# Kernel optimization log

Measured on AMD Instinct MI355X. Metric: run time of the kernel, lower is better.

## Reference

```python
import jax, jax.numpy as jnp
import numpy as np

D_MODEL = 256; N_HEADS = 8; N_LEVELS = 4; N_POINTS = 4
D_HEAD = D_MODEL // N_HEADS


def setup_inputs() -> dict:
    key = jax.random.key(0)
    ks = jax.random.split(key, 8)
    N, Lq = 4, 4096
    shapes = np.array([4096, 2048, 1024, 512], dtype=np.int32)  # temporal lengths per level
    Len_in = int(shapes.sum())  # 7680
    start = np.concatenate([[0], np.cumsum(shapes)[:-1]]).astype(np.int32)
    HLP = N_HEADS * N_LEVELS * N_POINTS
    return {
        "query": jax.random.normal(ks[0], (N, Lq, D_MODEL), jnp.float32),
        "reference_points": jax.random.uniform(ks[1], (N, Lq, N_LEVELS, 1), jnp.float32),
        "input_flatten": jax.random.normal(ks[2], (N, Len_in, D_MODEL), jnp.float32),
        "input_spatial_shapes": jnp.asarray(shapes),
        "input_level_start_index": jnp.asarray(start),
        "W_off": jax.random.normal(ks[3], (D_MODEL, HLP), jnp.float32) * 0.01,
        "b_off": jax.random.normal(ks[4], (HLP,), jnp.float32) * 2.0,
        "W_aw": jax.random.normal(ks[5], (D_MODEL, HLP), jnp.float32) * 0.02,
        "b_aw": jnp.zeros((HLP,), jnp.float32),
        "W_v": jax.random.normal(ks[6], (D_MODEL, D_MODEL), jnp.float32) / np.sqrt(D_MODEL).astype(np.float32),
        "b_v": jnp.zeros((D_MODEL,), jnp.float32),
        "W_out": jax.random.normal(ks[7], (D_MODEL, D_MODEL), jnp.float32) / np.sqrt(D_MODEL).astype(np.float32),
        "b_out": jnp.zeros((D_MODEL,), jnp.float32),
    }


def reference(query, reference_points, input_flatten, input_spatial_shapes,
              input_level_start_index, W_off, b_off, W_aw, b_aw, W_v, b_v,
              W_out, b_out):
    N, Lq, C = query.shape
    M, L, P, Dh = N_HEADS, N_LEVELS, N_POINTS, D_HEAD
    S = input_flatten.shape[1]

    value = (input_flatten @ W_v + b_v).reshape(N, S, M, Dh)
    off = (query @ W_off + b_off).reshape(N, Lq, M, L, P)
    aw = jax.nn.softmax((query @ W_aw + b_aw).reshape(N, Lq, M, L * P), axis=-1)
    aw = aw.reshape(N, Lq, M, L, P)

    # reference_points last dim == 1 branch: loc = ref + off / T_l, in [0,1]
    T = input_spatial_shapes.astype(jnp.float32)[None, None, None, :, None]  # [1,1,1,L,1]
    loc = reference_points[:, :, None, :, None, 0] + off / T  # [N,Lq,M,L,P]

    # grid_sample(align_corners=False, padding_mode='border') along W with H=1, y=0.5:
    # pixel coord x = loc*T - 0.5, clamped to [0, T-1], then linear interp.
    x = jnp.clip(loc * T - 0.5, 0.0, T - 1.0)
    x0 = jnp.floor(x)
    w1 = x - x0                                   # frac weight for right neighbor
    i0 = x0.astype(jnp.int32)
    i1 = jnp.minimum(i0 + 1, input_spatial_shapes[None, None, None, :, None] - 1)
    base = input_level_start_index[None, None, None, :, None]
    g0 = i0 + base                                # global flattened indices [N,Lq,M,L,P]
    g1 = i1 + base

    v = value.transpose(0, 2, 1, 3)               # [N,M,S,Dh]

    def gather(idx):
        idxt = idx.transpose(0, 2, 1, 3, 4).reshape(N, M, Lq * L * P, 1)
        return jnp.take_along_axis(v, idxt, axis=2).reshape(N, M, Lq, L, P, Dh)

    s0 = gather(g0)
    s1 = gather(g1)
    w1t = w1.transpose(0, 2, 1, 3, 4)[..., None]   # [N,M,Lq,L,P,1]
    samp = s0 * (1.0 - w1t) + s1 * w1t             # [N,M,Lq,L,P,Dh]

    awt = aw.transpose(0, 2, 1, 3, 4)[..., None]
    out = (samp * awt).sum(axis=(3, 4))            # [N,M,Lq,Dh]
    out = out.transpose(0, 2, 1, 3).reshape(N, Lq, M * Dh)
    return out @ W_out + b_out
```

## Files before the change

kernel.cpp:

```cpp
#include <hip/hip_runtime.h>
#include <hip/hip_bf16.h>
#include <cstddef>
#include <cstdint>

#define D_MODEL   256
#define N_HEADS   8
#define N_LEVELS  4
#define N_POINTS  4
#define D_HEAD    32
#define HLP       128
#define NBATCH    4
#define LQ        4096
#define S_LEN     7680

typedef __attribute__((ext_vector_type(8))) short  short8;
typedef __attribute__((ext_vector_type(4))) float  f32x4;
typedef __attribute__((ext_vector_type(8))) unsigned short ushort8;

__device__ __forceinline__ unsigned short f2bf(float x) {
    __hip_bfloat16 h = __float2bfloat16(x);
    return *reinterpret_cast<unsigned short*>(&h);
}
__device__ __forceinline__ float bf2f(unsigned short u) {
    unsigned int v = ((unsigned int)u) << 16;
    return *reinterpret_cast<float*>(&v);
}

__device__ __forceinline__ void gload_lds16(const void* g, void* l) {
    __builtin_amdgcn_global_load_lds(
        (const __attribute__((address_space(1))) void*)g,
        (__attribute__((address_space(3))) void*)l,
        16, 0, 0);
}

__global__ __launch_bounds__(256) void conv_bf16_kernel(
    const float* __restrict__ src, unsigned short* __restrict__ dst, int n)
{
    size_t i = ((size_t)blockIdx.x * blockDim.x + threadIdx.x) * 8;
    if (i >= (size_t)n) return;
    float4 a = *(const float4*)(src + i);
    float4 b = *(const float4*)(src + i + 4);
    ushort8 r;
    r[0] = f2bf(a.x); r[1] = f2bf(a.y); r[2] = f2bf(a.z); r[3] = f2bf(a.w);
    r[4] = f2bf(b.x); r[5] = f2bf(b.y); r[6] = f2bf(b.z); r[7] = f2bf(b.w);
    *(ushort8*)(dst + i) = r;
}

__global__ __launch_bounds__(256) void transpose_w_kernel(
    const float* __restrict__ src, unsigned short* __restrict__ dst, int N)
{
    __shared__ float t[64][65];
    const int k0 = blockIdx.y * 64, n0 = blockIdx.x * 64;
    const int tid = threadIdx.x;
    #pragma unroll
    for (int i = 0; i < 16; ++i) {
        int idx = tid + i * 256;
        int kk = idx >> 6, nn = idx & 63;
        t[kk][nn] = src[(size_t)(k0 + kk) * N + n0 + nn];
    }
    __syncthreads();
    #pragma unroll
    for (int i = 0; i < 16; ++i) {
        int idx = tid + i * 256;
        int nn = idx >> 6, kk = idx & 63;
        dst[(size_t)(n0 + nn) * 256 + k0 + kk] = f2bf(t[kk][nn]);
    }
}

__global__ void bias_cat_kernel(const float* __restrict__ b0,
                                const float* __restrict__ b1,
                                float* __restrict__ out)
{
    int t = threadIdx.x;
    out[t] = (t < 128) ? b0[t] : b1[t - 128];
}

template <bool BF16_OUT>
__global__ __launch_bounds__(256) void mfma_gemm_kernel(
    const unsigned short* __restrict__ A,
    const unsigned short* __restrict__ Bt,
    const float* __restrict__ bias,
    void* __restrict__ Cout, int M)
{
    __shared__ unsigned short Als[8][64][8];
    __shared__ unsigned short Bls[8][64][8];

    const int tid  = threadIdx.x;
    const int lane = tid & 63;
    const int w    = tid >> 6;
    const int wm   = w & 1;
    const int wn   = w >> 1;
    const int row0 = blockIdx.y * 128;
    const int col0 = blockIdx.x * 128;

    const int lr = (lane & 15);
    const int lk = (lane >> 4) * 8;

    f32x4 acc[4][4] = {};

    for (int kt = 0; kt < 8; ++kt) {
        const int k0 = kt * 32;
        #pragma unroll
        for (int c = 0; c < 2; ++c) {
            const int im = w * 2 + c;
            const size_t ga = (size_t)(row0 + im * 16 + lr) * 256 + k0 + lk;
            gload_lds16(A + ga, &Als[im][0][0]);
            const int in = w * 2 + c;
            const size_t gb = (size_t)(col0 + in * 16 + lr) * 256 + k0 + lk;
            gload_lds16(Bt + gb, &Bls[in][0][0]);
        }
        __syncthreads();

        short8 af[4], bfr[4];
        #pragma unroll
        for (int i = 0; i < 4; ++i) af[i]  = *(const short8*)&Als[wm * 4 + i][lane][0];
        #pragma unroll
        for (int j = 0; j < 4; ++j) bfr[j] = *(const short8*)&Bls[wn * 4 + j][lane][0];

        #pragma unroll
        for (int i = 0; i < 4; ++i)
            #pragma unroll
            for (int j = 0; j < 4; ++j)
                acc[i][j] = __builtin_amdgcn_mfma_f32_16x16x32_bf16(
                    af[i], bfr[j], acc[i][j], 0, 0, 0);
        __syncthreads();
    }

    const int r0 = row0 + wm * 64;
    const int c0 = col0 + wn * 64;
    const int prow = (lane >> 4) * 4;
    const int pcol = lane & 15;
    #pragma unroll
    for (int j = 0; j < 4; ++j) {
        const int col = c0 + j * 16 + pcol;
        const float bs = bias[col];
        #pragma unroll
        for (int i = 0; i < 4; ++i) {
            #pragma unroll
            for (int r = 0; r < 4; ++r) {
                const int row = r0 + i * 16 + prow + r;
                const float v = acc[i][j][r] + bs;
                if (BF16_OUT)
                    ((unsigned short*)Cout)[(size_t)row * 256 + col] = f2bf(v);
                else
                    ((float*)Cout)[(size_t)row * 256 + col] = v;
            }
        }
    }
}

__global__ __launch_bounds__(128) void sample_kernel(
    const float* __restrict__ P, const float* __restrict__ refp,
    const int* __restrict__ shapes, const int* __restrict__ lstart,
    const unsigned short* __restrict__ value, unsigned short* __restrict__ tout)
{
    __shared__ int   sg0[HLP];
    __shared__ int   sg1[HLP];
    __shared__ float sw[HLP];
    __shared__ float se[HLP];
    __shared__ float smax[N_HEADS];
    __shared__ float srsum[N_HEADS];

    const int nq  = blockIdx.x;
    const int n   = nq >> 12;
    const int tid = threadIdx.x;

    {
        const int l = (tid >> 2) & 3;
        const float off   = P[(size_t)nq * 256 + tid];
        const float logit = P[(size_t)nq * 256 + 128 + tid];
        const float T     = (float)shapes[l];
        const float ref   = refp[(size_t)nq * N_LEVELS + l];
        float x = ref * T + off - 0.5f;
        x = fminf(fmaxf(x, 0.0f), T - 1.0f);
        const float x0 = floorf(x);
        const int   i0 = (int)x0;
        const int   i1 = min(i0 + 1, shapes[l] - 1);
        const int   base = lstart[l];
        sg0[tid] = i0 + base;
        sg1[tid] = i1 + base;
        sw[tid]  = x - x0;
        se[tid]  = logit;
    }
    __syncthreads();
    if (tid < N_HEADS) {
        float mx = -1e30f;
        #pragma unroll
        for (int i = 0; i < 16; ++i) mx = fmaxf(mx, se[tid * 16 + i]);
        smax[tid] = mx;
    }
    __syncthreads();
    se[tid] = __expf(se[tid] - smax[tid >> 4]);
    __syncthreads();
    if (tid < N_HEADS) {
        float s = 0.f;
        #pragma unroll
        for (int i = 0; i < 16; ++i) s += se[tid * 16 + i];
        srsum[tid] = 1.0f / s;
    }
    __syncthreads();

    const int m  = tid >> 4;
    const int dp = tid & 15;
    const float rs = srsum[m];
    const unsigned short* vbase = value + (size_t)n * S_LEN * 256 + m * 32 + 2 * dp;

    float acc0 = 0.f, acc1 = 0.f;
    #pragma unroll
    for (int i = 0; i < 16; ++i) {
        const int j = m * 16 + i;
        const float a = se[j] * rs;
        const float ww = sw[j];
        const unsigned int u0 = *(const unsigned int*)(vbase + (size_t)sg0[j] * 256);
        const unsigned int u1 = *(const unsigned int*)(vbase + (size_t)sg1[j] * 256);
        const float v0a = bf2f((unsigned short)(u0 & 0xffff));
        const float v0b = bf2f((unsigned short)(u0 >> 16));
        const float v1a = bf2f((unsigned short)(u1 & 0xffff));
        const float v1b = bf2f((unsigned short)(u1 >> 16));
        acc0 += a * (v0a + ww * (v1a - v0a));
        acc1 += a * (v0b + ww * (v1b - v0b));
    }
    unsigned int out = (unsigned int)f2bf(acc0) | ((unsigned int)f2bf(acc1) << 16);
    *(unsigned int*)(tout + (size_t)nq * 256 + 2 * tid) = out;
}

extern "C" void kernel_launch(void* const* d_in, const int* in_sizes, int n_in,
                              void* d_out, int out_size, void* d_ws, size_t ws_size,
                              hipStream_t stream)
{
    const float* query  = (const float*)d_in[0];
    const float* refp   = (const float*)d_in[1];
    const float* inflat = (const float*)d_in[2];
    const int*   shapes = (const int*)d_in[3];
    const int*   lstart = (const int*)d_in[4];
    const float* W_off  = (const float*)d_in[5];
    const float* b_off  = (const float*)d_in[6];
    const float* W_aw   = (const float*)d_in[7];
    const float* b_aw   = (const float*)d_in[8];
    const float* W_v    = (const float*)d_in[9];
    const float* b_v    = (const float*)d_in[10];
    const float* W_out  = (const float*)d_in[11];
    const float* b_out  = (const float*)d_in[12];

    const int M_val = NBATCH * S_LEN;
    const int M_q   = NBATCH * LQ;
    const int n_val = M_val * D_MODEL;
    const int n_q   = M_q * D_MODEL;

    char* p = (char*)d_ws;
    unsigned short* value_bf  = (unsigned short*)p; p += (size_t)n_val * 2;
    float*          P         = (float*)p;          p += (size_t)M_q * 256 * 4;
    unsigned short* inflat_bf = (unsigned short*)p; p += (size_t)n_val * 2;
    unsigned short* query_bf  = (unsigned short*)p; p += (size_t)n_q * 2;
    unsigned short* tbuf      = query_bf;
    unsigned short* Wv_t      = (unsigned short*)p; p += 256 * 256 * 2;
    unsigned short* Wcat_t    = (unsigned short*)p; p += 256 * 256 * 2;
    unsigned short* Wout_t    = (unsigned short*)p; p += 256 * 256 * 2;
    float*          bcat      = (float*)p;          p += 256 * 4;

    conv_bf16_kernel<<<(n_val / 8 + 255) / 256, 256, 0, stream>>>(inflat, inflat_bf, n_val);
    conv_bf16_kernel<<<(n_q / 8 + 255) / 256, 256, 0, stream>>>(query, query_bf, n_q);
    transpose_w_kernel<<<dim3(4, 4), 256, 0, stream>>>(W_v, Wv_t, 256);
    transpose_w_kernel<<<dim3(2, 4), 256, 0, stream>>>(W_off, Wcat_t, 128);
    transpose_w_kernel<<<dim3(2, 4), 256, 0, stream>>>(W_aw, Wcat_t + 128 * 256, 128);
    transpose_w_kernel<<<dim3(4, 4), 256, 0, stream>>>(W_out, Wout_t, 256);
    bias_cat_kernel<<<1, 256, 0, stream>>>(b_off, b_aw, bcat);

    mfma_gemm_kernel<true><<<dim3(2, M_val / 128), 256, 0, stream>>>(
        inflat_bf, Wv_t, b_v, value_bf, M_val);
    mfma_gemm_kernel<false><<<dim3(2, M_q / 128), 256, 0, stream>>>(
        query_bf, Wcat_t, bcat, P, M_q);
    sample_kernel<<<M_q, 128, 0, stream>>>(P, refp, shapes, lstart, value_bf, tbuf);
    mfma_gemm_kernel<false><<<dim3(2, M_q / 128), 256, 0, stream>>>(
        tbuf, Wout_t, b_out, (float*)d_out, M_q);
}
```

Measured before the change: 180.1 us.

## Fuse fp32-to-bf16 conversion into GEMMs, merge prep kernels, restructure sampling

The separate fp32-to-bf16 conversion passes over input_flatten and query are dropped. The GEMM now loads fp32 A rows directly, converts them in registers and stores them to LDS. The weight transposes and bias concat are merged into one prep launch. The sample kernel now handles 8 queries per 256-thread block, each thread doing 16-byte vector gathers of 8 channels, and blocks are remapped so each XCD works on one batch's value tensor. This removes two full memory passes and several launches, at the cost of synchronous fp32 A loads in the GEMM that replace async global-to-LDS copies.

```diff
diff --git a/kernel.cpp b/kernel.cpp
--- a/kernel.cpp
+++ b/kernel.cpp
@@ -33,30 +33,30 @@
         16, 0, 0);
 }
 
-__global__ __launch_bounds__(256) void conv_bf16_kernel(
-    const float* __restrict__ src, unsigned short* __restrict__ dst, int n)
-{
-    size_t i = ((size_t)blockIdx.x * blockDim.x + threadIdx.x) * 8;
-    if (i >= (size_t)n) return;
-    float4 a = *(const float4*)(src + i);
-    float4 b = *(const float4*)(src + i + 4);
-    ushort8 r;
-    r[0] = f2bf(a.x); r[1] = f2bf(a.y); r[2] = f2bf(a.z); r[3] = f2bf(a.w);
-    r[4] = f2bf(b.x); r[5] = f2bf(b.y); r[6] = f2bf(b.z); r[7] = f2bf(b.w);
-    *(ushort8*)(dst + i) = r;
-}
-
-__global__ __launch_bounds__(256) void transpose_w_kernel(
-    const float* __restrict__ src, unsigned short* __restrict__ dst, int N)
+__global__ __launch_bounds__(256) void prep_kernel(
+    const float* __restrict__ W_v,  const float* __restrict__ W_off,
+    const float* __restrict__ W_aw, const float* __restrict__ W_out,
+    const float* __restrict__ b_off, const float* __restrict__ b_aw,
+    unsigned short* __restrict__ Wv_t, unsigned short* __restrict__ Wcat_t,
+    unsigned short* __restrict__ Wout_t, float* __restrict__ bcat)
 {
     __shared__ float t[64][65];
-    const int k0 = blockIdx.y * 64, n0 = blockIdx.x * 64;
+    const int z   = blockIdx.z;
+    const int k0  = blockIdx.y * 64;
+    const int n0  = blockIdx.x * 64;
     const int tid = threadIdx.x;
+
+    const float* src; int srcN; int cs; unsigned short* dst;
+    if (z == 0)      { src = W_v;   srcN = 256; cs = n0;       dst = Wv_t;  }
+    else if (z == 2) { src = W_out; srcN = 256; cs = n0;       dst = Wout_t;}
+    else if (n0 < 128){ src = W_off; srcN = 128; cs = n0;      dst = Wcat_t;}
+    else             { src = W_aw;  srcN = 128; cs = n0 - 128; dst = Wcat_t;}
+
     #pragma unroll
     for (int i = 0; i < 16; ++i) {
         int idx = tid + i * 256;
         int kk = idx >> 6, nn = idx & 63;
-        t[kk][nn] = src[(size_t)(k0 + kk) * N + n0 + nn];
+        t[kk][nn] = src[(size_t)(k0 + kk) * srcN + cs + nn];
     }
     __syncthreads();
     #pragma unroll
@@ -65,25 +65,20 @@
         int nn = idx >> 6, kk = idx & 63;
         dst[(size_t)(n0 + nn) * 256 + k0 + kk] = f2bf(t[kk][nn]);
     }
-}
-
-__global__ void bias_cat_kernel(const float* __restrict__ b0,
-                                const float* __restrict__ b1,
-                                float* __restrict__ out)
-{
-    int t = threadIdx.x;
-    out[t] = (t < 128) ? b0[t] : b1[t - 128];
-}
-
-template <bool BF16_OUT>
+    if (z == 1 && blockIdx.x == 0 && blockIdx.y == 0) {
+        bcat[tid] = (tid < 128) ? b_off[tid] : b_aw[tid - 128];
+    }
+}
+
+template <bool A_FP32, bool BF16_OUT>
 __global__ __launch_bounds__(256) void mfma_gemm_kernel(
-    const unsigned short* __restrict__ A,
+    const void* __restrict__ Aptr,
     const unsigned short* __restrict__ Bt,
     const float* __restrict__ bias,
     void* __restrict__ Cout, int M)
 {
-    __shared__ unsigned short Als[8][64][8];
-    __shared__ unsigned short Bls[8][64][8];
+    __shared__ alignas(16) unsigned short Als[8][64][8];
+    __shared__ alignas(16) unsigned short Bls[8][64][8];
 
     const int tid  = threadIdx.x;
     const int lane = tid & 63;
@@ -103,11 +98,24 @@
         #pragma unroll
         for (int c = 0; c < 2; ++c) {
             const int im = w * 2 + c;
-            const size_t ga = (size_t)(row0 + im * 16 + lr) * 256 + k0 + lk;
-            gload_lds16(A + ga, &Als[im][0][0]);
-            const int in = w * 2 + c;
-            const size_t gb = (size_t)(col0 + in * 16 + lr) * 256 + k0 + lk;
-            gload_lds16(Bt + gb, &Bls[in][0][0]);
+            if (A_FP32) {
+                const float* Af = (const float*)Aptr;
+                const float* ap = Af + (size_t)(row0 + im * 16 + lr) * 256 + k0 + lk;
+                const float4 a0 = *(const float4*)(ap);
+                const float4 a1 = *(const float4*)(ap + 4);
+                short8 pk;
+                pk[0] = (short)f2bf(a0.x); pk[1] = (short)f2bf(a0.y);
+                pk[2] = (short)f2bf(a0.z); pk[3] = (short)f2bf(a0.w);
+                pk[4] = (short)f2bf(a1.x); pk[5] = (short)f2bf(a1.y);
+                pk[6] = (short)f2bf(a1.z); pk[7] = (short)f2bf(a1.w);
+                *(short8*)&Als[im][lane][0] = pk;
+            } else {
+                const unsigned short* Ab = (const unsigned short*)Aptr;
+                const size_t ga = (size_t)(row0 + im * 16 + lr) * 256 + k0 + lk;
+                gload_lds16(Ab + ga, &Als[im][0][0]);
+            }
+            const size_t gb = (size_t)(col0 + im * 16 + lr) * 256 + k0 + lk;
+            gload_lds16(Bt + gb, &Bls[im][0][0]);
         }
         __syncthreads();
 
@@ -149,26 +157,33 @@
     }
 }
 
-__global__ __launch_bounds__(128) void sample_kernel(
+__global__ __launch_bounds__(256) void sample_kernel(
     const float* __restrict__ P, const float* __restrict__ refp,
     const int* __restrict__ shapes, const int* __restrict__ lstart,
     const unsigned short* __restrict__ value, unsigned short* __restrict__ tout)
 {
-    __shared__ int   sg0[HLP];
-    __shared__ int   sg1[HLP];
-    __shared__ float sw[HLP];
-    __shared__ float se[HLP];
-    __shared__ float smax[N_HEADS];
-    __shared__ float srsum[N_HEADS];
-
-    const int nq  = blockIdx.x;
-    const int n   = nq >> 12;
-    const int tid = threadIdx.x;
-
-    {
-        const int l = (tid >> 2) & 3;
-        const float off   = P[(size_t)nq * 256 + tid];
-        const float logit = P[(size_t)nq * 256 + 128 + tid];
+    __shared__ int   sG0[8][HLP];
+    __shared__ int   sG1[8][HLP];
+    __shared__ float sW [8][HLP];
+    __shared__ float sA [8][HLP];
+
+    const int b    = blockIdx.x;
+    const int xcd  = b & 7;
+    const int slot = b >> 3;
+    const int n    = xcd >> 1;
+    const int qg   = (slot << 1) | (xcd & 1);
+    const int nq0  = n * LQ + qg * 8;
+    const int tid  = threadIdx.x;
+
+    #pragma unroll
+    for (int i = 0; i < 4; ++i) {
+        const int idx = tid + i * 256;
+        const int q   = idx >> 7;
+        const int j   = idx & 127;
+        const int l   = (j >> 2) & 3;
+        const int nq  = nq0 + q;
+        const float off   = P[(size_t)nq * 256 + j];
+        const float logit = P[(size_t)nq * 256 + 128 + j];
         const float T     = (float)shapes[l];
         const float ref   = refp[(size_t)nq * N_LEVELS + l];
         float x = ref * T + off - 0.5f;
@@ -177,51 +192,54 @@
         const int   i0 = (int)x0;
         const int   i1 = min(i0 + 1, shapes[l] - 1);
         const int   base = lstart[l];
-        sg0[tid] = i0 + base;
-        sg1[tid] = i1 + base;
-        sw[tid]  = x - x0;
-        se[tid]  = logit;
+        sG0[q][j] = i0 + base;
+        sG1[q][j] = i1 + base;
+        sW [q][j] = x - x0;
+        sA [q][j] = logit;
     }
     __syncthreads();
-    if (tid < N_HEADS) {
+
+    if (tid < 64) {
+        const int q = tid >> 3;
+        const int m = tid & 7;
+        float e[16];
         float mx = -1e30f;
         #pragma unroll
-        for (int i = 0; i < 16; ++i) mx = fmaxf(mx, se[tid * 16 + i]);
-        smax[tid] = mx;
+        for (int i = 0; i < 16; ++i) { e[i] = sA[q][m * 16 + i]; mx = fmaxf(mx, e[i]); }
+        float s = 0.f;
+        #pragma unroll
+        for (int i = 0; i < 16; ++i) { e[i] = __expf(e[i] - mx); s += e[i]; }
+        const float rs = 1.0f / s;
+        #pragma unroll
+        for (int i = 0; i < 16; ++i) sA[q][m * 16 + i] = e[i] * rs;
     }
     __syncthreads();
-    se[tid] = __expf(se[tid] - smax[tid >> 4]);
-    __syncthreads();
-    if (tid < N_HEADS) {
-        float s = 0.f;
-        #pragma unroll
-        for (int i = 0; i < 16; ++i) s += se[tid * 16 + i];
-        srsum[tid] = 1.0f / s;
-    }
-    __syncthreads();
-
-    const int m  = tid >> 4;
-    const int dp = tid & 15;
-    const float rs = srsum[m];
-    const unsigned short* vbase = value + (size_t)n * S_LEN * 256 + m * 32 + 2 * dp;
-
-    float acc0 = 0.f, acc1 = 0.f;
+
+    const int q  = tid >> 5;
+    const int r  = tid & 31;
+    const int m  = r >> 2;
+    const int ql = r & 3;
+    const unsigned short* vb = value + (size_t)n * S_LEN * 256 + m * 32 + ql * 8;
+
+    float acc[8] = {};
     #pragma unroll
     for (int i = 0; i < 16; ++i) {
         const int j = m * 16 + i;
-        const float a = se[j] * rs;
-        const float ww = sw[j];
-        const unsigned int u0 = *(const unsigned int*)(vbase + (size_t)sg0[j] * 256);
-        const unsigned int u1 = *(const unsigned int*)(vbase + (size_t)sg1[j] * 256);
-        const float v0a = bf2f((unsigned short)(u0 & 0xffff));
-        const float v0b = bf2f((unsigned short)(u0 >> 16));
-        const float v1a = bf2f((unsigned short)(u1 & 0xffff));
-        const float v1b = bf2f((unsigned short)(u1 >> 16));
-        acc0 += a * (v0a + ww * (v1a - v0a));
-        acc1 += a * (v0b + ww * (v1b - v0b));
-    }
-    unsigned int out = (unsigned int)f2bf(acc0) | ((unsigned int)f2bf(acc1) << 16);
-    *(unsigned int*)(tout + (size_t)nq * 256 + 2 * tid) = out;
+        const float a  = sA[q][j];
+        const float ww = sW[q][j];
+        const ushort8 u0 = *(const ushort8*)(vb + (size_t)sG0[q][j] * 256);
+        const ushort8 u1 = *(const ushort8*)(vb + (size_t)sG1[q][j] * 256);
+        #pragma unroll
+        for (int d = 0; d < 8; ++d) {
+            const float v0 = bf2f(u0[d]);
+            const float v1 = bf2f(u1[d]);
+            acc[d] += a * (v0 + ww * (v1 - v0));
+        }
+    }
+    ushort8 o;
+    #pragma unroll
+    for (int d = 0; d < 8; ++d) o[d] = f2bf(acc[d]);
+    *(ushort8*)(tout + (size_t)(nq0 + q) * 256 + r * 8) = o;
 }
 
 extern "C" void kernel_launch(void* const* d_in, const int* in_sizes, int n_in,
@@ -244,33 +262,24 @@
 
     const int M_val = NBATCH * S_LEN;
     const int M_q   = NBATCH * LQ;
-    const int n_val = M_val * D_MODEL;
-    const int n_q   = M_q * D_MODEL;
 
     char* p = (char*)d_ws;
-    unsigned short* value_bf  = (unsigned short*)p; p += (size_t)n_val * 2;
-    float*          P         = (float*)p;          p += (size_t)M_q * 256 * 4;
-    unsigned short* inflat_bf = (unsigned short*)p; p += (size_t)n_val * 2;
-    unsigned short* query_bf  = (unsigned short*)p; p += (size_t)n_q * 2;
-    unsigned short* tbuf      = query_bf;
-    unsigned short* Wv_t      = (unsigned short*)p; p += 256 * 256 * 2;
-    unsigned short* Wcat_t    = (unsigned short*)p; p += 256 * 256 * 2;
-    unsigned short* Wout_t    = (unsigned short*)p; p += 256 * 256 * 2;
-    float*          bcat      = (float*)p;          p += 256 * 4;
-
-    conv_bf16_kernel<<<(n_val / 8 + 255) / 256, 256, 0, stream>>>(inflat, inflat_bf, n_val);
-    conv_bf16_kernel<<<(n_q / 8 + 255) / 256, 256, 0, stream>>>(query, query_bf, n_q);
-    transpose_w_kernel<<<dim3(4, 4), 256, 0, stream>>>(W_v, Wv_t, 256);
-    transpose_w_kernel<<<dim3(2, 4), 256, 0, stream>>>(W_off, Wcat_t, 128);
-    transpose_w_kernel<<<dim3(2, 4), 256, 0, stream>>>(W_aw, Wcat_t + 128 * 256, 128);
-    transpose_w_kernel<<<dim3(4, 4), 256, 0, stream>>>(W_out, Wout_t, 256);
-    bias_cat_kernel<<<1, 256, 0, stream>>>(b_off, b_aw, bcat);
-
-    mfma_gemm_kernel<true><<<dim3(2, M_val / 128), 256, 0, stream>>>(
-        inflat_bf, Wv_t, b_v, value_bf, M_val);
-    mfma_gemm_kernel<false><<<dim3(2, M_q / 128), 256, 0, stream>>>(
-        query_bf, Wcat_t, bcat, P, M_q);
-    sample_kernel<<<M_q, 128, 0, stream>>>(P, refp, shapes, lstart, value_bf, tbuf);
-    mfma_gemm_kernel<false><<<dim3(2, M_q / 128), 256, 0, stream>>>(
+    unsigned short* value_bf = (unsigned short*)p; p += (size_t)M_val * D_MODEL * 2;
+    float*          P        = (float*)p;          p += (size_t)M_q * 256 * 4;
+    unsigned short* tbuf     = (unsigned short*)p; p += (size_t)M_q * D_MODEL * 2;
+    unsigned short* Wv_t     = (unsigned short*)p; p += 256 * 256 * 2;
+    unsigned short* Wcat_t   = (unsigned short*)p; p += 256 * 256 * 2;
+    unsigned short* Wout_t   = (unsigned short*)p; p += 256 * 256 * 2;
+    float*          bcat     = (float*)p;          p += 256 * 4;
+
+    prep_kernel<<<dim3(4, 4, 3), 256, 0, stream>>>(
+        W_v, W_off, W_aw, W_out, b_off, b_aw, Wv_t, Wcat_t, Wout_t, bcat);
+    mfma_gemm_kernel<true, true><<<dim3(2, M_val / 128), 256, 0, stream>>>(
+        inflat, Wv_t, b_v, value_bf, M_val);
+    mfma_gemm_kernel<true, false><<<dim3(2, M_q / 128), 256, 0, stream>>>(
+        query, Wcat_t, bcat, P, M_q);
+    sample_kernel<<<M_q / 8, 256, 0, stream>>>(
+        P, refp, shapes, lstart, value_bf, tbuf);
+    mfma_gemm_kernel<false, false><<<dim3(2, M_q / 128), 256, 0, stream>>>(
         tbuf, Wout_t, b_out, (float*)d_out, M_q);
 }
```

New measurement: 173.7 us. 3.6% less time.
